# Performance work log

Measured on AMD Instinct MI355X. Metric: run time of the kernel, lower is better.

The kernel has to match this reference:

```python
import jax, jax.numpy as jnp
import numpy as np

B, S, T = 32, 50, 50
V_SRC, V_TRG = 32000, 32000
E, H, A = 128, 128, 128


def setup_inputs() -> dict:
    key = jax.random.key(0)
    ks = jax.random.split(key, 24)
    g = lambda k, shape, s=0.08: jax.random.normal(k, shape, dtype=jnp.float32) * s
    inp = {
        'src': jax.random.randint(ks[0], (B, S), 0, V_SRC, dtype=jnp.int32),
        'trg': jax.random.randint(ks[1], (B, T), 0, V_TRG, dtype=jnp.int32),
        'emb_src': g(ks[2], (V_SRC, E)),
        'emb_trg': g(ks[3], (V_TRG, E)),
        # PyTorch LSTM params: gates ordered (i, f, g, o)
        'enc_Wih': g(ks[4], (4 * H, E)), 'enc_Whh': g(ks[5], (4 * H, H)),
        'enc_bih': g(ks[6], (4 * H,)), 'enc_bhh': g(ks[7], (4 * H,)),
        'dec_Wih': g(ks[8], (4 * H, E)), 'dec_Whh': g(ks[9], (4 * H, H)),
        'dec_bih': g(ks[10], (4 * H,)), 'dec_bhh': g(ks[11], (4 * H,)),
        'att_w1s': g(ks[12], (A, H)), 'att_b1s': g(ks[13], (A,)),
        'att_w1t': g(ks[14], (A, H)), 'att_b1t': g(ks[15], (A,)),
        'att_w2': g(ks[16], (1, A)), 'att_b2': g(ks[17], (1,)),
        'out_w': g(ks[18], (H, 2 * H)), 'out_b': g(ks[19], (H,)),
        'sm_w': g(ks[20], (V_TRG, H)), 'sm_b': g(ks[21], (V_TRG,)),
    }
    return inp


def _lstm_cell(x, h, c, Wih, Whh, bih, bhh):
    gates = x @ Wih.T + bih + h @ Whh.T + bhh  # [B, 4H]
    i, f, g, o = jnp.split(gates, 4, axis=-1)
    c_new = jax.nn.sigmoid(f) * c + jax.nn.sigmoid(i) * jnp.tanh(g)
    h_new = jax.nn.sigmoid(o) * jnp.tanh(c_new)
    return h_new, c_new


def reference(src, trg, emb_src, emb_trg,
              enc_Wih, enc_Whh, enc_bih, enc_bhh,
              dec_Wih, dec_Whh, dec_bih, dec_bhh,
              att_w1s, att_b1s, att_w1t, att_b1t, att_w2, att_b2,
              out_w, out_b, sm_w, sm_b):
    batch = src.shape[0]
    hidden = enc_Whh.shape[1]
    h0 = jnp.zeros((batch, hidden), dtype=emb_src.dtype)
    c0 = jnp.zeros((batch, hidden), dtype=emb_src.dtype)

    # ---- encoder LSTM over src ----
    x_src = emb_src[src]                      # [B,S,E]
    def enc_step(carry, x_t):
        h, c = carry
        h, c = _lstm_cell(x_t, h, c, enc_Wih, enc_Whh, enc_bih, enc_bhh)
        return (h, c), h
    _, enc_out = jax.lax.scan(enc_step, (h0, c0), x_src.transpose(1, 0, 2))
    enc_out = enc_out.transpose(1, 0, 2)      # [B,S,H]

    # att_w1_src(src_vectors) is constant across decode steps
    att_src = enc_out @ att_w1s.T + att_b1s   # [B,S,A]

    # ---- decoder (init_hidden = zeros, per original forward) ----
    x_trg = emb_trg[trg[:, :-1]]              # [B,T-1,E]
    def dec_step(carry, x_t):
        h, c = carry
        h, c = _lstm_cell(x_t, h, c, dec_Wih, dec_Whh, dec_bih, dec_bhh)
        att_tgt = h @ att_w1t.T + att_b1t                       # [B,A]
        comb = jnp.tanh(att_src + att_tgt[:, None, :])          # [B,S,A]
        scores = (comb @ att_w2.T + att_b2)[..., 0]             # [B,S]
        align = jax.nn.softmax(scores, axis=1)
        att_vec = jnp.einsum('bs,bsh->bh', align, enc_out)      # [B,H]
        final = jnp.tanh(jnp.concatenate([h, att_vec], axis=1) @ out_w.T + out_b)
        logits = final @ sm_w.T + sm_b                          # [B,V]
        return (h, c), logits
    _, logits = jax.lax.scan(dec_step, (h0, c0), x_trg.transpose(1, 0, 2))
    return logits.transpose(1, 0, 2)          # [B,T-1,V]
```

## Files before the change

kernel.cpp:

```cpp
#include <hip/hip_runtime.h>

typedef unsigned short ushort_t;
typedef __attribute__((ext_vector_type(2))) float f32x2;
typedef __attribute__((ext_vector_type(8))) short bfrag;
typedef __attribute__((ext_vector_type(4))) float f32x4;

__device__ __forceinline__ float sigf(float x) { return 1.0f / (1.0f + __expf(-x)); }
__device__ __forceinline__ float tanhf_fast(float x) { return 1.0f - 2.0f / (__expf(2.0f * x) + 1.0f); }
__device__ __forceinline__ ushort_t f2bf(float f) {
    unsigned u = __float_as_uint(f);
    unsigned r = (u + 0x7fffu + ((u >> 16) & 1u)) >> 16;
    return (ushort_t)r;
}

__global__ void prep_kernel(const float* __restrict__ eW, float* __restrict__ eWT,
                            const float* __restrict__ dW, float* __restrict__ dWT,
                            const float* __restrict__ w1s, float* __restrict__ w1sT,
                            const float* __restrict__ w1t, float* __restrict__ w1tT,
                            const float* __restrict__ ow, float* __restrict__ owT,
                            const float* __restrict__ smw, ushort_t* __restrict__ smwbf)
{
    int bid = blockIdx.x;
    int tid = threadIdx.x;
    if (bid >= 192) {
        int i = ((bid - 192) * 256 + tid) * 4;
        float4 v = *(const float4*)(smw + i);
        smwbf[i + 0] = f2bf(v.x);
        smwbf[i + 1] = f2bf(v.y);
        smwbf[i + 2] = f2bf(v.z);
        smwbf[i + 3] = f2bf(v.w);
        return;
    }
    __shared__ float tile[32][33];
    const float* in; float* outp; int C; int t;
    if (bid < 64)       { in = eW;  outp = eWT;  C = 128; t = bid; }
    else if (bid < 128) { in = dW;  outp = dWT;  C = 128; t = bid - 64; }
    else if (bid < 144) { in = w1s; outp = w1sT; C = 128; t = bid - 128; }
    else if (bid < 160) { in = w1t; outp = w1tT; C = 128; t = bid - 144; }
    else                { in = ow;  outp = owT;  C = 256; t = bid - 160; }
    int R = (bid < 128) ? 512 : 128;
    int gx = C >> 5;
    int c0 = (t & (gx - 1)) * 32, r0 = (t / gx) * 32;
    int x = tid & 31, y = tid >> 5;
#pragma unroll
    for (int i = 0; i < 32; i += 8)
        tile[y + i][x] = in[(r0 + y + i) * C + c0 + x];
    __syncthreads();
#pragma unroll
    for (int i = 0; i < 32; i += 8)
        outp[(c0 + y + i) * R + r0 + x] = tile[x][y + i];
}

__device__ __forceinline__ void tok_gemv_body(const float* __restrict__ X,
                                              const int* __restrict__ toks,
                                              int divv,
                                              const float* __restrict__ WT,
                                              const float* __restrict__ b1,
                                              const float* __restrict__ b2,
                                              float* __restrict__ out,
                                              int ntok, int n0, int J, float* xs)
{
    for (int i = threadIdx.x; i < 4 * 128; i += J) {
        int tt = i >> 7, k = i & 127;
        int n = n0 + tt;
        if (n >= ntok) n = ntok - 1;
        int row;
        if (!toks) row = n;
        else if (divv == 0) row = toks[n];
        else { int bb = n / divv; int t = n - bb * divv; row = toks[bb * (divv + 1) + t]; }
        xs[i] = X[row * 128 + k];
    }
    __syncthreads();
    int j = threadIdx.x;
    float bias = b1[j] + (b2 ? b2[j] : 0.0f);
    const float4* x0 = (const float4*)(xs);
    const float4* x1 = (const float4*)(xs + 128);
    const float4* x2 = (const float4*)(xs + 256);
    const float4* x3 = (const float4*)(xs + 384);
    float a0 = 0.f, a1 = 0.f, a2 = 0.f, a3 = 0.f;
#pragma unroll 8
    for (int k4 = 0; k4 < 32; ++k4) {
        float4 v0 = x0[k4], v1 = x1[k4], v2 = x2[k4], v3 = x3[k4];
        float w0 = WT[(k4 * 4 + 0) * J + j];
        float w1 = WT[(k4 * 4 + 1) * J + j];
        float w2_ = WT[(k4 * 4 + 2) * J + j];
        float w3 = WT[(k4 * 4 + 3) * J + j];
        a0 += v0.x * w0 + v0.y * w1 + v0.z * w2_ + v0.w * w3;
        a1 += v1.x * w0 + v1.y * w1 + v1.z * w2_ + v1.w * w3;
        a2 += v2.x * w0 + v2.y * w1 + v2.z * w2_ + v2.w * w3;
        a3 += v3.x * w0 + v3.y * w1 + v3.z * w2_ + v3.w * w3;
    }
    float accs[4] = {a0, a1, a2, a3};
#pragma unroll
    for (int tt = 0; tt < 4; ++tt) {
        int n = n0 + tt;
        if (n < ntok) out[n * J + j] = bias + accs[tt];
    }
}

__global__ void tok_gemv_kernel(const float* __restrict__ X,
                                const int* __restrict__ toks, int divv,
                                const float* __restrict__ WT,
                                const float* __restrict__ b1,
                                const float* __restrict__ b2,
                                float* __restrict__ out, int ntok)
{
    __shared__ __align__(16) float xs[4 * 128];
    tok_gemv_body(X, toks, divv, WT, b1, b2, out, ntok, blockIdx.x * 4, blockDim.x, xs);
}

__global__ void tok_gemv2_kernel(const float* __restrict__ embS, const int* __restrict__ src,
                                 const float* __restrict__ WTe,
                                 const float* __restrict__ bihE, const float* __restrict__ bhhE,
                                 float* __restrict__ gihE,
                                 const float* __restrict__ embT, const int* __restrict__ trg,
                                 const float* __restrict__ WTd,
                                 const float* __restrict__ bihD, const float* __restrict__ bhhD,
                                 float* __restrict__ gihD)
{
    __shared__ __align__(16) float xs[4 * 128];
    if (blockIdx.x < 400)
        tok_gemv_body(embS, src, 0, WTe, bihE, bhhE, gihE, 1600, blockIdx.x * 4, blockDim.x, xs);
    else
        tok_gemv_body(embT, trg, 49, WTd, bihD, bhhD, gihD, 1568, (blockIdx.x - 400) * 4, blockDim.x, xs);
}

__global__ void __launch_bounds__(512, 2) rnn_kernel(const float* __restrict__ gih_enc,
                                                     const float* __restrict__ enc_Whh,
                                                     const float* __restrict__ gih_dec,
                                                     const float* __restrict__ dec_Whh,
                                                     float* __restrict__ enc_out,
                                                     float* __restrict__ hdec)
{
    bool is_enc = blockIdx.x < 32;
    int b = is_enc ? blockIdx.x : blockIdx.x - 32;
    int T = is_enc ? 50 : 49;
    const float* gih = is_enc ? gih_enc : gih_dec;
    const float* Whh = is_enc ? enc_Whh : dec_Whh;
    float* hout = is_enc ? enc_out : hdec;

    int tid = threadIdx.x;
    __shared__ __align__(16) float h[128];
    __shared__ float gates[512];

    f32x2 w2[64];
    const f32x2* wr = (const f32x2*)(Whh + tid * 128);
#pragma unroll
    for (int k = 0; k < 64; ++k) w2[k] = wr[k];

    float c = 0.f;
    if (tid < 128) h[tid] = 0.f;
    const float* gb = gih + b * T * 512 + tid;
    float gnext = gb[0];
    const f32x2* h2 = (const f32x2*)h;

    for (int t = 0; t < T; ++t) {
        __syncthreads();
        float g0 = gnext;
        if (t + 1 < T) gnext = gb[(t + 1) * 512];
        f32x2 s0 = {0.f, 0.f}, s1 = {0.f, 0.f};
#pragma unroll
        for (int k = 0; k < 64; k += 2) {
            s0 += h2[k] * w2[k];
            s1 += h2[k + 1] * w2[k + 1];
        }
        gates[tid] = g0 + s0.x + s0.y + s1.x + s1.y;
        __syncthreads();
        if (tid < 128) {
            float gi = gates[tid], gf = gates[128 + tid], gg = gates[256 + tid], go = gates[384 + tid];
            c = sigf(gf) * c + sigf(gi) * tanhf_fast(gg);
            float hn = sigf(go) * tanhf_fast(c);
            h[tid] = hn;
            hout[(b * T + t) * 128 + tid] = hn;
        }
    }
}

__global__ void __launch_bounds__(128) att_par_kernel(const float* __restrict__ hdec,
                                                      const float* __restrict__ att_src,
                                                      const float* __restrict__ enc_out,
                                                      const float* __restrict__ w1tT,
                                                      const float* __restrict__ b1t,
                                                      const float* __restrict__ w2,
                                                      const float* __restrict__ b2,
                                                      const float* __restrict__ out_wT,
                                                      const float* __restrict__ out_b,
                                                      ushort_t* __restrict__ fin_bf)
{
    int t = blockIdx.x, b = blockIdx.y;
    int tid = threadIdx.x, lane = tid & 63, wv = tid >> 6;
    __shared__ __align__(16) float h[128];
    __shared__ __align__(16) float attv[128];
    __shared__ float attt[128];
    __shared__ float sc[64];

    h[tid] = hdec[(b * 49 + t) * 128 + tid];
    __syncthreads();
    const float4* h4 = (const float4*)h;

    {
        float acc = b1t[tid];
#pragma unroll
        for (int k4 = 0; k4 < 32; ++k4) {
            float4 hv = h4[k4];
            int k = k4 * 4;
            acc += hv.x * w1tT[(k + 0) * 128 + tid] + hv.y * w1tT[(k + 1) * 128 + tid]
                 + hv.z * w1tT[(k + 2) * 128 + tid] + hv.w * w1tT[(k + 3) * 128 + tid];
        }
        attt[tid] = acc;
    }
    __syncthreads();
    {
        float w2a = w2[lane], w2b = w2[lane + 64], b2s = b2[0];
        float ta = attt[lane], tb = attt[lane + 64];
        const float* asb = att_src + b * 6400;
        for (int s = wv; s < 50; s += 2) {
            float v = w2a * tanhf_fast(asb[s * 128 + lane] + ta)
                    + w2b * tanhf_fast(asb[s * 128 + 64 + lane] + tb);
#pragma unroll
            for (int off = 32; off; off >>= 1) v += __shfl_down(v, off);
            if (lane == 0) sc[s] = v + b2s;
        }
    }
    __syncthreads();
    if (tid < 64) {
        float x = (tid < 50) ? sc[tid] : -1e30f;
        float m = x;
#pragma unroll
        for (int off = 32; off; off >>= 1) m = fmaxf(m, __shfl_xor(m, off));
        float e = (tid < 50) ? __expf(x - m) : 0.f;
        float ssum = e;
#pragma unroll
        for (int off = 32; off; off >>= 1) ssum += __shfl_xor(ssum, off);
        if (tid < 50) sc[tid] = e / ssum;
    }
    __syncthreads();
    {
        const float* eob = enc_out + b * 6400;
        float av = 0.f;
        for (int s = 0; s < 50; ++s) av += sc[s] * eob[s * 128 + tid];
        attv[tid] = av;
    }
    __syncthreads();
    {
        const float4* av4 = (const float4*)attv;
        float a3 = out_b[tid];
#pragma unroll
        for (int k4 = 0; k4 < 32; ++k4) {
            float4 hv = h4[k4];
            int k = k4 * 4;
            a3 += hv.x * out_wT[(k + 0) * 128 + tid] + hv.y * out_wT[(k + 1) * 128 + tid]
                + hv.z * out_wT[(k + 2) * 128 + tid] + hv.w * out_wT[(k + 3) * 128 + tid];
        }
#pragma unroll
        for (int k4 = 0; k4 < 32; ++k4) {
            float4 vv = av4[k4];
            int k = 128 + k4 * 4;
            a3 += vv.x * out_wT[(k + 0) * 128 + tid] + vv.y * out_wT[(k + 1) * 128 + tid]
                + vv.z * out_wT[(k + 2) * 128 + tid] + vv.w * out_wT[(k + 3) * 128 + tid];
        }
        fin_bf[(b * 49 + t) * 128 + tid] = f2bf(tanhf_fast(a3));
    }
}

__global__ void __launch_bounds__(256) logits_gemm_kernel(const ushort_t* __restrict__ A,
                                                          const ushort_t* __restrict__ Bw,
                                                          const float* __restrict__ bias,
                                                          float* __restrict__ out)
{
    int wv = threadIdx.x >> 6, lane = threadIdx.x & 63;
    int r = lane & 15, kq = (lane >> 4) * 8;
    int mbase = blockIdx.y * 64;
    int nb = blockIdx.x * 128 + wv * 32;

    bfrag a[4][4];
#pragma unroll
    for (int mt = 0; mt < 4; ++mt) {
        const ushort_t* ap = A + (mbase + mt * 16 + r) * 128 + kq;
#pragma unroll
        for (int kk = 0; kk < 4; ++kk) a[mt][kk] = *(const bfrag*)(ap + kk * 32);
    }
    bfrag bf[2][4];
#pragma unroll
    for (int vt = 0; vt < 2; ++vt) {
        const ushort_t* bp = Bw + (nb + vt * 16 + r) * 128 + kq;
#pragma unroll
        for (int kk = 0; kk < 4; ++kk) bf[vt][kk] = *(const bfrag*)(bp + kk * 32);
    }

#pragma unroll
    for (int mt = 0; mt < 4; ++mt) {
        bool valid = (mbase + mt * 16) < 1568;
#pragma unroll
        for (int vt = 0; vt < 2; ++vt) {
            f32x4 acc = {0.f, 0.f, 0.f, 0.f};
            acc = __builtin_amdgcn_mfma_f32_16x16x32_bf16(bf[vt][0], a[mt][0], acc, 0, 0, 0);
            acc = __builtin_amdgcn_mfma_f32_16x16x32_bf16(bf[vt][1], a[mt][1], acc, 0, 0, 0);
            acc = __builtin_amdgcn_mfma_f32_16x16x32_bf16(bf[vt][2], a[mt][2], acc, 0, 0, 0);
            acc = __builtin_amdgcn_mfma_f32_16x16x32_bf16(bf[vt][3], a[mt][3], acc, 0, 0, 0);
            if (valid) {
                int m = mbase + mt * 16 + r;
                int col = nb + vt * 16 + (lane >> 4) * 4;
                float4 bs = *(const float4*)(bias + col);
                float4 st = {acc[0] + bs.x, acc[1] + bs.y, acc[2] + bs.z, acc[3] + bs.w};
                *(float4*)(out + (size_t)m * 32000 + col) = st;
            }
        }
    }
}

extern "C" void kernel_launch(void* const* d_in, const int* in_sizes, int n_in,
                              void* d_out, int out_size, void* d_ws, size_t ws_size,
                              hipStream_t stream)
{
    const int* src      = (const int*)d_in[0];
    const int* trg      = (const int*)d_in[1];
    const float* emb_src = (const float*)d_in[2];
    const float* emb_trg = (const float*)d_in[3];
    const float* enc_Wih = (const float*)d_in[4];
    const float* enc_Whh = (const float*)d_in[5];
    const float* enc_bih = (const float*)d_in[6];
    const float* enc_bhh = (const float*)d_in[7];
    const float* dec_Wih = (const float*)d_in[8];
    const float* dec_Whh = (const float*)d_in[9];
    const float* dec_bih = (const float*)d_in[10];
    const float* dec_bhh = (const float*)d_in[11];
    const float* att_w1s = (const float*)d_in[12];
    const float* att_b1s = (const float*)d_in[13];
    const float* att_w1t = (const float*)d_in[14];
    const float* att_b1t = (const float*)d_in[15];
    const float* att_w2  = (const float*)d_in[16];
    const float* att_b2  = (const float*)d_in[17];
    const float* out_w   = (const float*)d_in[18];
    const float* out_b   = (const float*)d_in[19];
    const float* sm_w    = (const float*)d_in[20];
    const float* sm_b    = (const float*)d_in[21];
    float* out = (float*)d_out;

    char* ws = (char*)d_ws;
    float*    gih_enc = (float*)(ws);
    float*    att_src = (float*)(ws);
    float*    gih_dec = (float*)(ws + 3276800);
    ushort_t* fin_bf  = (ushort_t*)(ws + 3276800);
    float*    enc_out = (float*)(ws + 6488064);
    float*    hdec    = (float*)(ws + 7307264);
    ushort_t* smw_bf  = (ushort_t*)(ws + 8110080);
    float*    WihT_e  = (float*)(ws + 16302080);
    float*    WihT_d  = (float*)(ws + 16564224);
    float*    w1sT    = (float*)(ws + 16826368);
    float*    w1tT    = (float*)(ws + 16891904);
    float*    outwT   = (float*)(ws + 16957440);

    prep_kernel<<<4192, 256, 0, stream>>>(enc_Wih, WihT_e, dec_Wih, WihT_d,
                                          att_w1s, w1sT, att_w1t, w1tT,
                                          out_w, outwT, sm_w, smw_bf);

    tok_gemv2_kernel<<<792, 512, 0, stream>>>(emb_src, src, WihT_e, enc_bih, enc_bhh, gih_enc,
                                              emb_trg, trg, WihT_d, dec_bih, dec_bhh, gih_dec);

    rnn_kernel<<<64, 512, 0, stream>>>(gih_enc, enc_Whh, gih_dec, dec_Whh, enc_out, hdec);

    tok_gemv_kernel<<<400, 128, 0, stream>>>(enc_out, nullptr, 0, w1sT, att_b1s, nullptr, att_src, 1600);

    att_par_kernel<<<dim3(49, 32), 128, 0, stream>>>(hdec, att_src, enc_out,
                                                     w1tT, att_b1t, att_w2, att_b2,
                                                     outwT, out_b, fin_bf);

    logits_gemm_kernel<<<dim3(250, 25), 256, 0, stream>>>(fin_bf, smw_bf, sm_b, out);
}
```

Baseline: 457.9 us.

## Fuse sm_w bf16 conversion into logits GEMM, batch attention steps, precompute gate activations

The separate pass that converts sm_w to bf16 is removed. The logits GEMM now loads fp32 sm_w and converts it in registers, with each wave keeping one 16-column B tile resident and looping over all 98 M tiles while prefetching A. The attention kernel handles two timesteps per block so weight loads are shared. The LSTM kernel applies the gate nonlinearities across all 512 threads before the cell update and reads h as float4. The trade-off is a longer serial M loop per wave, fewer blocks for latency hiding, and an odd final block that recomputes t=48.

```diff
diff --git a/kernel.cpp b/kernel.cpp
--- a/kernel.cpp
+++ b/kernel.cpp
@@ -17,20 +17,10 @@
                             const float* __restrict__ dW, float* __restrict__ dWT,
                             const float* __restrict__ w1s, float* __restrict__ w1sT,
                             const float* __restrict__ w1t, float* __restrict__ w1tT,
-                            const float* __restrict__ ow, float* __restrict__ owT,
-                            const float* __restrict__ smw, ushort_t* __restrict__ smwbf)
+                            const float* __restrict__ ow, float* __restrict__ owT)
 {
     int bid = blockIdx.x;
     int tid = threadIdx.x;
-    if (bid >= 192) {
-        int i = ((bid - 192) * 256 + tid) * 4;
-        float4 v = *(const float4*)(smw + i);
-        smwbf[i + 0] = f2bf(v.x);
-        smwbf[i + 1] = f2bf(v.y);
-        smwbf[i + 2] = f2bf(v.z);
-        smwbf[i + 3] = f2bf(v.w);
-        return;
-    }
     __shared__ float tile[32][33];
     const float* in; float* outp; int C; int t;
     if (bid < 64)       { in = eW;  outp = eWT;  C = 128; t = bid; }
@@ -143,16 +133,17 @@
     __shared__ __align__(16) float h[128];
     __shared__ float gates[512];
 
-    f32x2 w2[64];
-    const f32x2* wr = (const f32x2*)(Whh + tid * 128);
-#pragma unroll
-    for (int k = 0; k < 64; ++k) w2[k] = wr[k];
+    float4 w4[32];
+    const float4* wr = (const float4*)(Whh + tid * 128);
+#pragma unroll
+    for (int k = 0; k < 32; ++k) w4[k] = wr[k];
 
     float c = 0.f;
     if (tid < 128) h[tid] = 0.f;
     const float* gb = gih + b * T * 512 + tid;
     float gnext = gb[0];
-    const f32x2* h2 = (const f32x2*)h;
+    const float4* h4 = (const float4*)h;
+    int gt = tid >> 7;
 
     for (int t = 0; t < T; ++t) {
         __syncthreads();
@@ -160,16 +151,20 @@
         if (t + 1 < T) gnext = gb[(t + 1) * 512];
         f32x2 s0 = {0.f, 0.f}, s1 = {0.f, 0.f};
 #pragma unroll
-        for (int k = 0; k < 64; k += 2) {
-            s0 += h2[k] * w2[k];
-            s1 += h2[k + 1] * w2[k + 1];
-        }
-        gates[tid] = g0 + s0.x + s0.y + s1.x + s1.y;
+        for (int k = 0; k < 32; ++k) {
+            float4 hv = h4[k];
+            f32x2 ha = {hv.x, hv.y}, hb = {hv.z, hv.w};
+            f32x2 wa = {w4[k].x, w4[k].y}, wb = {w4[k].z, w4[k].w};
+            s0 += ha * wa;
+            s1 += hb * wb;
+        }
+        float acc = g0 + s0.x + s0.y + s1.x + s1.y;
+        gates[tid] = (gt == 2) ? tanhf_fast(acc) : sigf(acc);
         __syncthreads();
         if (tid < 128) {
-            float gi = gates[tid], gf = gates[128 + tid], gg = gates[256 + tid], go = gates[384 + tid];
-            c = sigf(gf) * c + sigf(gi) * tanhf_fast(gg);
-            float hn = sigf(go) * tanhf_fast(c);
+            float ai = gates[tid], af = gates[128 + tid], ag = gates[256 + tid], ao = gates[384 + tid];
+            c = af * c + ai * ag;
+            float hn = ao * tanhf_fast(c);
             h[tid] = hn;
             hout[(b * T + t) * 128 + tid] = hn;
         }
@@ -187,125 +182,153 @@
                                                       const float* __restrict__ out_b,
                                                       ushort_t* __restrict__ fin_bf)
 {
-    int t = blockIdx.x, b = blockIdx.y;
+    int b = blockIdx.y;
+    int t0 = blockIdx.x * 2;
+    int t1 = t0 + 1; if (t1 > 48) t1 = 48;
     int tid = threadIdx.x, lane = tid & 63, wv = tid >> 6;
-    __shared__ __align__(16) float h[128];
-    __shared__ __align__(16) float attv[128];
-    __shared__ float attt[128];
-    __shared__ float sc[64];
-
-    h[tid] = hdec[(b * 49 + t) * 128 + tid];
-    __syncthreads();
-    const float4* h4 = (const float4*)h;
-
-    {
-        float acc = b1t[tid];
+    __shared__ __align__(16) float h0[128], h1[128];
+    __shared__ __align__(16) float av0s[128], av1s[128];
+    __shared__ float attt0[128], attt1[128];
+    __shared__ float sc0[64], sc1[64];
+
+    h0[tid] = hdec[(b * 49 + t0) * 128 + tid];
+    h1[tid] = hdec[(b * 49 + t1) * 128 + tid];
+    __syncthreads();
+    const float4* h04 = (const float4*)h0;
+    const float4* h14 = (const float4*)h1;
+
+    {
+        float acc0 = b1t[tid], acc1 = acc0;
 #pragma unroll
         for (int k4 = 0; k4 < 32; ++k4) {
-            float4 hv = h4[k4];
+            float4 hv0 = h04[k4], hv1 = h14[k4];
             int k = k4 * 4;
-            acc += hv.x * w1tT[(k + 0) * 128 + tid] + hv.y * w1tT[(k + 1) * 128 + tid]
-                 + hv.z * w1tT[(k + 2) * 128 + tid] + hv.w * w1tT[(k + 3) * 128 + tid];
-        }
-        attt[tid] = acc;
+            float wA = w1tT[(k + 0) * 128 + tid], wB = w1tT[(k + 1) * 128 + tid];
+            float wC = w1tT[(k + 2) * 128 + tid], wD = w1tT[(k + 3) * 128 + tid];
+            acc0 += hv0.x * wA + hv0.y * wB + hv0.z * wC + hv0.w * wD;
+            acc1 += hv1.x * wA + hv1.y * wB + hv1.z * wC + hv1.w * wD;
+        }
+        attt0[tid] = acc0; attt1[tid] = acc1;
     }
     __syncthreads();
     {
         float w2a = w2[lane], w2b = w2[lane + 64], b2s = b2[0];
-        float ta = attt[lane], tb = attt[lane + 64];
+        float ta0 = attt0[lane], tb0 = attt0[lane + 64];
+        float ta1 = attt1[lane], tb1 = attt1[lane + 64];
         const float* asb = att_src + b * 6400;
         for (int s = wv; s < 50; s += 2) {
-            float v = w2a * tanhf_fast(asb[s * 128 + lane] + ta)
-                    + w2b * tanhf_fast(asb[s * 128 + 64 + lane] + tb);
-#pragma unroll
-            for (int off = 32; off; off >>= 1) v += __shfl_down(v, off);
-            if (lane == 0) sc[s] = v + b2s;
-        }
-    }
-    __syncthreads();
-    if (tid < 64) {
-        float x = (tid < 50) ? sc[tid] : -1e30f;
+            float lo = asb[s * 128 + lane], hi = asb[s * 128 + 64 + lane];
+            float v0 = w2a * tanhf_fast(lo + ta0) + w2b * tanhf_fast(hi + tb0);
+            float v1 = w2a * tanhf_fast(lo + ta1) + w2b * tanhf_fast(hi + tb1);
+#pragma unroll
+            for (int off = 32; off; off >>= 1) {
+                v0 += __shfl_down(v0, off);
+                v1 += __shfl_down(v1, off);
+            }
+            if (lane == 0) { sc0[s] = v0 + b2s; sc1[s] = v1 + b2s; }
+        }
+    }
+    __syncthreads();
+    {
+        float* scp = wv ? sc1 : sc0;
+        float x = (lane < 50) ? scp[lane] : -1e30f;
         float m = x;
 #pragma unroll
         for (int off = 32; off; off >>= 1) m = fmaxf(m, __shfl_xor(m, off));
-        float e = (tid < 50) ? __expf(x - m) : 0.f;
+        float e = (lane < 50) ? __expf(x - m) : 0.f;
         float ssum = e;
 #pragma unroll
         for (int off = 32; off; off >>= 1) ssum += __shfl_xor(ssum, off);
-        if (tid < 50) sc[tid] = e / ssum;
+        if (lane < 50) scp[lane] = e / ssum;
     }
     __syncthreads();
     {
         const float* eob = enc_out + b * 6400;
-        float av = 0.f;
-        for (int s = 0; s < 50; ++s) av += sc[s] * eob[s * 128 + tid];
-        attv[tid] = av;
-    }
-    __syncthreads();
-    {
-        const float4* av4 = (const float4*)attv;
-        float a3 = out_b[tid];
+        float a0 = 0.f, a1 = 0.f;
+        for (int s = 0; s < 50; ++s) {
+            float ev = eob[s * 128 + tid];
+            a0 += sc0[s] * ev; a1 += sc1[s] * ev;
+        }
+        av0s[tid] = a0; av1s[tid] = a1;
+    }
+    __syncthreads();
+    {
+        const float4* a04 = (const float4*)av0s;
+        const float4* a14 = (const float4*)av1s;
+        float f0 = out_b[tid], f1 = f0;
 #pragma unroll
         for (int k4 = 0; k4 < 32; ++k4) {
-            float4 hv = h4[k4];
+            float4 hv0 = h04[k4], hv1 = h14[k4];
             int k = k4 * 4;
-            a3 += hv.x * out_wT[(k + 0) * 128 + tid] + hv.y * out_wT[(k + 1) * 128 + tid]
-                + hv.z * out_wT[(k + 2) * 128 + tid] + hv.w * out_wT[(k + 3) * 128 + tid];
+            float wA = out_wT[(k + 0) * 128 + tid], wB = out_wT[(k + 1) * 128 + tid];
+            float wC = out_wT[(k + 2) * 128 + tid], wD = out_wT[(k + 3) * 128 + tid];
+            f0 += hv0.x * wA + hv0.y * wB + hv0.z * wC + hv0.w * wD;
+            f1 += hv1.x * wA + hv1.y * wB + hv1.z * wC + hv1.w * wD;
         }
 #pragma unroll
         for (int k4 = 0; k4 < 32; ++k4) {
-            float4 vv = av4[k4];
+            float4 v0 = a04[k4], v1 = a14[k4];
             int k = 128 + k4 * 4;
-            a3 += vv.x * out_wT[(k + 0) * 128 + tid] + vv.y * out_wT[(k + 1) * 128 + tid]
-                + vv.z * out_wT[(k + 2) * 128 + tid] + vv.w * out_wT[(k + 3) * 128 + tid];
-        }
-        fin_bf[(b * 49 + t) * 128 + tid] = f2bf(tanhf_fast(a3));
+            float wA = out_wT[(k + 0) * 128 + tid], wB = out_wT[(k + 1) * 128 + tid];
+            float wC = out_wT[(k + 2) * 128 + tid], wD = out_wT[(k + 3) * 128 + tid];
+            f0 += v0.x * wA + v0.y * wB + v0.z * wC + v0.w * wD;
+            f1 += v1.x * wA + v1.y * wB + v1.z * wC + v1.w * wD;
+        }
+        fin_bf[(b * 49 + t0) * 128 + tid] = f2bf(tanhf_fast(f0));
+        fin_bf[(b * 49 + t1) * 128 + tid] = f2bf(tanhf_fast(f1));
     }
 }
 
 __global__ void __launch_bounds__(256) logits_gemm_kernel(const ushort_t* __restrict__ A,
-                                                          const ushort_t* __restrict__ Bw,
+                                                          const float* __restrict__ Bw,
                                                           const float* __restrict__ bias,
                                                           float* __restrict__ out)
 {
     int wv = threadIdx.x >> 6, lane = threadIdx.x & 63;
     int r = lane & 15, kq = (lane >> 4) * 8;
-    int mbase = blockIdx.y * 64;
-    int nb = blockIdx.x * 128 + wv * 32;
-
-    bfrag a[4][4];
-#pragma unroll
-    for (int mt = 0; mt < 4; ++mt) {
-        const ushort_t* ap = A + (mbase + mt * 16 + r) * 128 + kq;
-#pragma unroll
-        for (int kk = 0; kk < 4; ++kk) a[mt][kk] = *(const bfrag*)(ap + kk * 32);
-    }
-    bfrag bf[2][4];
-#pragma unroll
-    for (int vt = 0; vt < 2; ++vt) {
-        const ushort_t* bp = Bw + (nb + vt * 16 + r) * 128 + kq;
-#pragma unroll
-        for (int kk = 0; kk < 4; ++kk) bf[vt][kk] = *(const bfrag*)(bp + kk * 32);
-    }
-
-#pragma unroll
-    for (int mt = 0; mt < 4; ++mt) {
-        bool valid = (mbase + mt * 16) < 1568;
-#pragma unroll
-        for (int vt = 0; vt < 2; ++vt) {
-            f32x4 acc = {0.f, 0.f, 0.f, 0.f};
-            acc = __builtin_amdgcn_mfma_f32_16x16x32_bf16(bf[vt][0], a[mt][0], acc, 0, 0, 0);
-            acc = __builtin_amdgcn_mfma_f32_16x16x32_bf16(bf[vt][1], a[mt][1], acc, 0, 0, 0);
-            acc = __builtin_amdgcn_mfma_f32_16x16x32_bf16(bf[vt][2], a[mt][2], acc, 0, 0, 0);
-            acc = __builtin_amdgcn_mfma_f32_16x16x32_bf16(bf[vt][3], a[mt][3], acc, 0, 0, 0);
-            if (valid) {
-                int m = mbase + mt * 16 + r;
-                int col = nb + vt * 16 + (lane >> 4) * 4;
-                float4 bs = *(const float4*)(bias + col);
-                float4 st = {acc[0] + bs.x, acc[1] + bs.y, acc[2] + bs.z, acc[3] + bs.w};
-                *(float4*)(out + (size_t)m * 32000 + col) = st;
-            }
-        }
+    int nb = blockIdx.x * 64 + wv * 16;
+
+    bfrag bf[4];
+    {
+        const float* bp = Bw + (size_t)(nb + r) * 128 + kq;
+#pragma unroll
+        for (int kk = 0; kk < 4; ++kk) {
+            float4 lo = *(const float4*)(bp + kk * 32);
+            float4 hi = *(const float4*)(bp + kk * 32 + 4);
+            bfrag f;
+            f[0] = (short)f2bf(lo.x); f[1] = (short)f2bf(lo.y);
+            f[2] = (short)f2bf(lo.z); f[3] = (short)f2bf(lo.w);
+            f[4] = (short)f2bf(hi.x); f[5] = (short)f2bf(hi.y);
+            f[6] = (short)f2bf(hi.z); f[7] = (short)f2bf(hi.w);
+            bf[kk] = f;
+        }
+    }
+    int colq = (lane >> 4) * 4;
+    float4 bs = *(const float4*)(bias + nb + colq);
+
+    const ushort_t* ab = A + r * 128 + kq;
+    bfrag a0 = *(const bfrag*)(ab);
+    bfrag a1 = *(const bfrag*)(ab + 32);
+    bfrag a2 = *(const bfrag*)(ab + 64);
+    bfrag a3 = *(const bfrag*)(ab + 96);
+
+    for (int mt = 0; mt < 98; ++mt) {
+        bfrag c0 = a0, c1 = a1, c2 = a2, c3 = a3;
+        if (mt < 97) {
+            const ushort_t* np = ab + (mt + 1) * 16 * 128;
+            a0 = *(const bfrag*)(np);
+            a1 = *(const bfrag*)(np + 32);
+            a2 = *(const bfrag*)(np + 64);
+            a3 = *(const bfrag*)(np + 96);
+        }
+        f32x4 acc = {0.f, 0.f, 0.f, 0.f};
+        acc = __builtin_amdgcn_mfma_f32_16x16x32_bf16(bf[0], c0, acc, 0, 0, 0);
+        acc = __builtin_amdgcn_mfma_f32_16x16x32_bf16(bf[1], c1, acc, 0, 0, 0);
+        acc = __builtin_amdgcn_mfma_f32_16x16x32_bf16(bf[2], c2, acc, 0, 0, 0);
+        acc = __builtin_amdgcn_mfma_f32_16x16x32_bf16(bf[3], c3, acc, 0, 0, 0);
+        int m = mt * 16 + r;
+        float4 st = {acc[0] + bs.x, acc[1] + bs.y, acc[2] + bs.z, acc[3] + bs.w};
+        *(float4*)(out + (size_t)m * 32000 + nb + colq) = st;
     }
 }
 
@@ -344,16 +367,15 @@
     ushort_t* fin_bf  = (ushort_t*)(ws + 3276800);
     float*    enc_out = (float*)(ws + 6488064);
     float*    hdec    = (float*)(ws + 7307264);
-    ushort_t* smw_bf  = (ushort_t*)(ws + 8110080);
-    float*    WihT_e  = (float*)(ws + 16302080);
-    float*    WihT_d  = (float*)(ws + 16564224);
-    float*    w1sT    = (float*)(ws + 16826368);
-    float*    w1tT    = (float*)(ws + 16891904);
-    float*    outwT   = (float*)(ws + 16957440);
-
-    prep_kernel<<<4192, 256, 0, stream>>>(enc_Wih, WihT_e, dec_Wih, WihT_d,
-                                          att_w1s, w1sT, att_w1t, w1tT,
-                                          out_w, outwT, sm_w, smw_bf);
+    float*    WihT_e  = (float*)(ws + 8110080);
+    float*    WihT_d  = (float*)(ws + 8372224);
+    float*    w1sT    = (float*)(ws + 8634368);
+    float*    w1tT    = (float*)(ws + 8699904);
+    float*    outwT   = (float*)(ws + 8765440);
+
+    prep_kernel<<<192, 256, 0, stream>>>(enc_Wih, WihT_e, dec_Wih, WihT_d,
+                                         att_w1s, w1sT, att_w1t, w1tT,
+                                         out_w, outwT);
 
     tok_gemv2_kernel<<<792, 512, 0, stream>>>(emb_src, src, WihT_e, enc_bih, enc_bhh, gih_enc,
                                               emb_trg, trg, WihT_d, dec_bih, dec_bhh, gih_dec);
@@ -362,9 +384,9 @@
 
     tok_gemv_kernel<<<400, 128, 0, stream>>>(enc_out, nullptr, 0, w1sT, att_b1s, nullptr, att_src, 1600);
 
-    att_par_kernel<<<dim3(49, 32), 128, 0, stream>>>(hdec, att_src, enc_out,
+    att_par_kernel<<<dim3(25, 32), 128, 0, stream>>>(hdec, att_src, enc_out,
                                                      w1tT, att_b1t, att_w2, att_b2,
                                                      outwT, out_b, fin_bf);
 
-    logits_gemm_kernel<<<dim3(250, 25), 256, 0, stream>>>(fin_bf, smw_bf, sm_b, out);
-}
+    logits_gemm_kernel<<<500, 256, 0, stream>>>(fin_bf, sm_w, sm_b, out);
+}
```

Result: faster. 438.7 us (-4.2%).
